# Optimization experiments

Hardware: AMD Instinct MI355X
Metric: run time of the kernel (lower is better)

Reference implementation:

```python
import jax, jax.numpy as jnp
import numpy as np

N, IN, OUT = 128, 1024, 1024
STE_TEMP = 1.0


def setup_inputs() -> dict:
    key = jax.random.key(0)
    k1, k2 = jax.random.split(key)
    x = jax.random.normal(k1, (N, IN), dtype=jnp.float32)
    # nn.init.uniform_(weight, -0.5, 0.5)
    weight = jax.random.uniform(k2, (OUT, IN), dtype=jnp.float32, minval=-0.5, maxval=0.5)
    bias = jnp.zeros((OUT,), dtype=jnp.float32)
    return {"x": x, "weight": weight, "bias": bias}


def reference(x, weight, bias):
    # scores: [N, out, in] = W[out,in] broadcast-added to x[N,1,in]
    scores = weight[None, :, :] + x[:, None, :]
    # training-mode forward: hard max value, STE blend with softmax-weighted smooth value
    hard = jnp.max(jax.lax.stop_gradient(scores), axis=-1)          # [N, out]
    soft_w = jax.nn.softmax(scores / STE_TEMP, axis=-1)              # [N, out, in]
    soft = jnp.sum(soft_w * scores, axis=-1)                          # [N, out]
    out = hard + (soft - jax.lax.stop_gradient(soft))
    return out + bias
```

## Files before the change

### kernel.cpp

```cpp
#include <hip/hip_runtime.h>

#define N_ROWS 128
#define IN_DIM 1024
#define OUT_DIM 1024


__global__ __launch_bounds__(256, 1)
void tropical_linear_kernel(const float* __restrict__ x,
                            const float* __restrict__ w,
                            const float* __restrict__ bias,
                            float* __restrict__ out) {
    __shared__ float4 xs[8 * 256];

    const int tid  = threadIdx.x;
    const int wid  = tid >> 6;
    const int lane = tid & 63;
    const int g    = lane & 15;
    const int og   = lane >> 4;

    const int bn = blockIdx.x >> 4;
    const int bo = blockIdx.x & 15;
    const int n0 = bn * 8;
    const int obase = bo * 64 + wid * 16 + og * 4;

    const float4* __restrict__ x4 = (const float4*)x;

    const float4* __restrict__ wp0 = (const float4*)w + (size_t)(obase + 0) * 256 + g;
    const float4* __restrict__ wp1 = (const float4*)w + (size_t)(obase + 1) * 256 + g;
    const float4* __restrict__ wp2 = (const float4*)w + (size_t)(obase + 2) * 256 + g;
    const float4* __restrict__ wp3 = (const float4*)w + (size_t)(obase + 3) * 256 + g;

#pragma unroll
    for (int i = 0; i < 8; ++i) {
        const int idx = tid + i * 256;
        xs[idx] = x4[(size_t)(n0 + (idx >> 8)) * 256 + (idx & 255)];
    }

    float4 wA[4], wB[4];
    wA[0] = wp0[0];  wA[1] = wp1[0];  wA[2] = wp2[0];  wA[3] = wp3[0];
    wB[0] = wp0[16]; wB[1] = wp1[16]; wB[2] = wp2[16]; wB[3] = wp3[16];

    float acc[8][4];
#pragma unroll
    for (int j = 0; j < 8; ++j)
#pragma unroll
        for (int r = 0; r < 4; ++r) acc[j][r] = -3.4e38f;

    __syncthreads();

    const float4* __restrict__ xsg = xs + g;

    float4 xA[8], xB[8];
#pragma unroll
    for (int j = 0; j < 8; ++j) xA[j] = xsg[j * 256];

#define TROPIC_STEP(WBUF, XBUF)                                   \
    _Pragma("unroll")                                             \
    for (int j = 0; j < 8; ++j) {                                 \
        const float4 xv = XBUF[j];                                \
        _Pragma("unroll")                                         \
        for (int r = 0; r < 4; ++r) {                             \
            const float s0 = WBUF[r].x + xv.x;                    \
            const float s1 = WBUF[r].y + xv.y;                    \
            const float s2 = WBUF[r].z + xv.z;                    \
            const float s3 = WBUF[r].w + xv.w;                    \
            const float m = fmaxf(fmaxf(s0, s1), s2);             \
            acc[j][r] = fmaxf(fmaxf(m, s3), acc[j][r]);           \
        }                                                         \
    }

#pragma unroll 1
    for (int tt = 0; tt < 7; ++tt) {
        const int t0 = 2 * tt;
#pragma unroll
        for (int j = 0; j < 8; ++j) xB[j] = xsg[j * 256 + (t0 + 1) * 16];
        TROPIC_STEP(wA, xA)
        wA[0] = wp0[(t0 + 2) * 16]; wA[1] = wp1[(t0 + 2) * 16];
        wA[2] = wp2[(t0 + 2) * 16]; wA[3] = wp3[(t0 + 2) * 16];
#pragma unroll
        for (int j = 0; j < 8; ++j) xA[j] = xsg[j * 256 + (t0 + 2) * 16];
        TROPIC_STEP(wB, xB)
        wB[0] = wp0[(t0 + 3) * 16]; wB[1] = wp1[(t0 + 3) * 16];
        wB[2] = wp2[(t0 + 3) * 16]; wB[3] = wp3[(t0 + 3) * 16];
    }
#pragma unroll
    for (int j = 0; j < 8; ++j) xB[j] = xsg[j * 256 + 15 * 16];
    TROPIC_STEP(wA, xA)
    TROPIC_STEP(wB, xB)

#undef TROPIC_STEP

    const int jj   = g & 7;
    const int half = g >> 3;
    float2 res = make_float2(0.f, 0.f);
#pragma unroll
    for (int j = 0; j < 8; ++j) {
#pragma unroll
        for (int r = 0; r < 4; ++r) {
            float v = acc[j][r];
            v = fmaxf(v, __shfl_xor(v, 1, 64));
            v = fmaxf(v, __shfl_xor(v, 2, 64));
            v = fmaxf(v, __shfl_xor(v, 4, 64));
            v = fmaxf(v, __shfl_xor(v, 8, 64));
            acc[j][r] = v;
        }
        if (jj == j) {
            res.x = half ? acc[j][2] : acc[j][0];
            res.y = half ? acc[j][3] : acc[j][1];
        }
    }
    const int oc = obase + half * 2;
    const float2 bv = *(const float2*)&bias[oc];
    res.x += bv.x;
    res.y += bv.y;
    *(float2*)&out[(size_t)(n0 + jj) * OUT_DIM + oc] = res;
}

extern "C" void kernel_launch(void* const* d_in, const int* in_sizes, int n_in,
                              void* d_out, int out_size, void* d_ws, size_t ws_size,
                              hipStream_t stream) {
    const float* x    = (const float*)d_in[0];
    const float* w    = (const float*)d_in[1];
    const float* bias = (const float*)d_in[2];
    float* out = (float*)d_out;

    dim3 grid(256);
    dim3 block(256);
    hipLaunchKernelGGL(tropical_linear_kernel, grid, block, 0, stream, x, w, bias, out);
}
```

Baseline: 72.24 us.

## Split reduction dimension across waves and quadruple grid size with LDS combine

Each block now covers 16 output columns instead of 64, and its four waves each handle a quarter of the input dimension. The per-wave partial maxima are combined through shared memory in a final step, and the grid grows from 256 to 1024 blocks with launch bounds raised to allow 4 blocks per CU. The aim is more parallelism and occupancy to fill the GPU's compute units. In exchange, each block reloads the full 8-row x tile for only 16 outputs (four times as much total x traffic), and it adds an extra barrier plus a shared-memory reduction.

```diff
diff --git a/kernel.cpp b/kernel.cpp
--- a/kernel.cpp
+++ b/kernel.cpp
@@ -5,12 +5,13 @@
 #define OUT_DIM 1024
 
 
-__global__ __launch_bounds__(256, 1)
+__global__ __launch_bounds__(256, 4)
 void tropical_linear_kernel(const float* __restrict__ x,
                             const float* __restrict__ w,
                             const float* __restrict__ bias,
                             float* __restrict__ out) {
     __shared__ float4 xs[8 * 256];
+    __shared__ float2 sc[4][64];
 
     const int tid  = threadIdx.x;
     const int wid  = tid >> 6;
@@ -18,23 +19,23 @@
     const int g    = lane & 15;
     const int og   = lane >> 4;
 
-    const int bn = blockIdx.x >> 4;
-    const int bo = blockIdx.x & 15;
+    const int bn = blockIdx.x >> 6;
+    const int bo = blockIdx.x & 63;
     const int n0 = bn * 8;
-    const int obase = bo * 64 + wid * 16 + og * 4;
+    const int obase = bo * 16 + og * 4;
 
     const float4* __restrict__ x4 = (const float4*)x;
-
-    const float4* __restrict__ wp0 = (const float4*)w + (size_t)(obase + 0) * 256 + g;
-    const float4* __restrict__ wp1 = (const float4*)w + (size_t)(obase + 1) * 256 + g;
-    const float4* __restrict__ wp2 = (const float4*)w + (size_t)(obase + 2) * 256 + g;
-    const float4* __restrict__ wp3 = (const float4*)w + (size_t)(obase + 3) * 256 + g;
 
 #pragma unroll
     for (int i = 0; i < 8; ++i) {
         const int idx = tid + i * 256;
         xs[idx] = x4[(size_t)(n0 + (idx >> 8)) * 256 + (idx & 255)];
     }
+
+    const float4* __restrict__ wp0 = (const float4*)w + (size_t)(obase + 0) * 256 + wid * 64 + g;
+    const float4* __restrict__ wp1 = (const float4*)w + (size_t)(obase + 1) * 256 + wid * 64 + g;
+    const float4* __restrict__ wp2 = (const float4*)w + (size_t)(obase + 2) * 256 + wid * 64 + g;
+    const float4* __restrict__ wp3 = (const float4*)w + (size_t)(obase + 3) * 256 + wid * 64 + g;
 
     float4 wA[4], wB[4];
     wA[0] = wp0[0];  wA[1] = wp1[0];  wA[2] = wp2[0];  wA[3] = wp3[0];
@@ -48,16 +49,14 @@
 
     __syncthreads();
 
-    const float4* __restrict__ xsg = xs + g;
+    const float4* __restrict__ xsg = xs + wid * 64 + g;
 
-    float4 xA[8], xB[8];
-#pragma unroll
-    for (int j = 0; j < 8; ++j) xA[j] = xsg[j * 256];
+    float4 xq[8];
 
-#define TROPIC_STEP(WBUF, XBUF)                                   \
+#define TROPIC_STEP(WBUF)                                         \
     _Pragma("unroll")                                             \
     for (int j = 0; j < 8; ++j) {                                 \
-        const float4 xv = XBUF[j];                                \
+        const float4 xv = xq[j];                                  \
         _Pragma("unroll")                                         \
         for (int r = 0; r < 4; ++r) {                             \
             const float s0 = WBUF[r].x + xv.x;                    \
@@ -69,30 +68,26 @@
         }                                                         \
     }
 
-#pragma unroll 1
-    for (int tt = 0; tt < 7; ++tt) {
-        const int t0 = 2 * tt;
 #pragma unroll
-        for (int j = 0; j < 8; ++j) xB[j] = xsg[j * 256 + (t0 + 1) * 16];
-        TROPIC_STEP(wA, xA)
-        wA[0] = wp0[(t0 + 2) * 16]; wA[1] = wp1[(t0 + 2) * 16];
-        wA[2] = wp2[(t0 + 2) * 16]; wA[3] = wp3[(t0 + 2) * 16];
+    for (int j = 0; j < 8; ++j) xq[j] = xsg[j * 256];
+    TROPIC_STEP(wA)
+    wA[0] = wp0[32]; wA[1] = wp1[32]; wA[2] = wp2[32]; wA[3] = wp3[32];
+
 #pragma unroll
-        for (int j = 0; j < 8; ++j) xA[j] = xsg[j * 256 + (t0 + 2) * 16];
-        TROPIC_STEP(wB, xB)
-        wB[0] = wp0[(t0 + 3) * 16]; wB[1] = wp1[(t0 + 3) * 16];
-        wB[2] = wp2[(t0 + 3) * 16]; wB[3] = wp3[(t0 + 3) * 16];
-    }
+    for (int j = 0; j < 8; ++j) xq[j] = xsg[j * 256 + 16];
+    TROPIC_STEP(wB)
+    wB[0] = wp0[48]; wB[1] = wp1[48]; wB[2] = wp2[48]; wB[3] = wp3[48];
+
 #pragma unroll
-    for (int j = 0; j < 8; ++j) xB[j] = xsg[j * 256 + 15 * 16];
-    TROPIC_STEP(wA, xA)
-    TROPIC_STEP(wB, xB)
+    for (int j = 0; j < 8; ++j) xq[j] = xsg[j * 256 + 32];
+    TROPIC_STEP(wA)
+
+#pragma unroll
+    for (int j = 0; j < 8; ++j) xq[j] = xsg[j * 256 + 48];
+    TROPIC_STEP(wB)
 
 #undef TROPIC_STEP
 
-    const int jj   = g & 7;
-    const int half = g >> 3;
-    float2 res = make_float2(0.f, 0.f);
 #pragma unroll
     for (int j = 0; j < 8; ++j) {
 #pragma unroll
@@ -104,16 +99,39 @@
             v = fmaxf(v, __shfl_xor(v, 8, 64));
             acc[j][r] = v;
         }
-        if (jj == j) {
-            res.x = half ? acc[j][2] : acc[j][0];
-            res.y = half ? acc[j][3] : acc[j][1];
+    }
+
+    {
+        const int jj = g >> 1;
+        const int pr = g & 1;
+        float2 res = make_float2(-3.4e38f, -3.4e38f);
+#pragma unroll
+        for (int j = 0; j < 8; ++j) {
+            if (jj == j) {
+                res.x = pr ? acc[j][2] : acc[j][0];
+                res.y = pr ? acc[j][3] : acc[j][1];
+            }
         }
+        sc[wid][og * 16 + g] = res;
     }
-    const int oc = obase + half * 2;
-    const float2 bv = *(const float2*)&bias[oc];
-    res.x += bv.x;
-    res.y += bv.y;
-    *(float2*)&out[(size_t)(n0 + jj) * OUT_DIM + oc] = res;
+    __syncthreads();
+
+    if (tid < 64) {
+        const int me  = tid;
+        float2 a = sc[0][me], b = sc[1][me], c = sc[2][me], d = sc[3][me];
+        float2 res;
+        res.x = fmaxf(fmaxf(a.x, b.x), fmaxf(c.x, d.x));
+        res.y = fmaxf(fmaxf(a.y, b.y), fmaxf(c.y, d.y));
+        const int ogf = me >> 4;
+        const int rem = me & 15;
+        const int j   = rem >> 1;
+        const int pr  = rem & 1;
+        const int o   = bo * 16 + ogf * 4 + pr * 2;
+        const float2 bv = *(const float2*)&bias[o];
+        res.x += bv.x;
+        res.y += bv.y;
+        *(float2*)&out[(size_t)(n0 + j) * OUT_DIM + o] = res;
+    }
 }
 
 extern "C" void kernel_launch(void* const* d_in, const int* in_sizes, int n_in,
@@ -124,7 +142,7 @@
     const float* bias = (const float*)d_in[2];
     float* out = (float*)d_out;
 
-    dim3 grid(256);
+    dim3 grid(1024);
     dim3 block(256);
     hipLaunchKernelGGL(tropical_linear_kernel, grid, block, 0, stream, x, w, bias, out);
 }
```

Result: slower. 86.26 us (+19.4%).
